# Kernel tuning notes

Measured on AMD Instinct MI355X. Metric: run time of the kernel, lower is better.

Reference implementation:

```python
import jax, jax.numpy as jnp
import numpy as np
from jax import lax

V, E, H, SEQ = 50257, 512, 512, 2048
TAGS, START, STOP = 12, 10, 11
NEG = -10000.0


def _lstm_dir(x, Wih, Whh, bih, bhh, reverse):
    # x: [T, in], Wih: [4H, in], Whh: [4H, H] (torch gate order i,f,g,o)
    h0 = jnp.zeros((Whh.shape[1],), x.dtype)
    c0 = jnp.zeros((Whh.shape[1],), x.dtype)
    b = bih + bhh

    def step(carry, xt):
        h, c = carry
        gates = Wih @ xt + Whh @ h + b  # [4H]
        i, f, g, o = jnp.split(gates, 4)
        c = jax.nn.sigmoid(f) * c + jax.nn.sigmoid(i) * jnp.tanh(g)
        h = jax.nn.sigmoid(o) * jnp.tanh(c)
        return (h, c), h

    _, hs = lax.scan(step, (h0, c0), x, reverse=reverse)
    return hs  # [T, H]


def _bilstm_layer(x, Wih, Whh, bih, bhh):
    # stacked params: leading dim 2 = (fwd, bwd)
    fwd = _lstm_dir(x, Wih[0], Whh[0], bih[0], bhh[0], False)
    bwd = _lstm_dir(x, Wih[1], Whh[1], bih[1], bhh[1], True)
    return jnp.concatenate([fwd, bwd], axis=-1)  # [T, 2H]


def _viterbi(feats, transitions):
    # feats: [T, TAGS]; transitions[next, prev]
    init = jnp.full((TAGS,), NEG, feats.dtype).at[START].set(0.0)

    def step(fv, feat):
        scores = fv[None, :] + transitions  # [next, prev]
        bptr = jnp.argmax(scores, axis=1)
        fv_new = jnp.max(scores, axis=1) + feat
        return fv_new, bptr

    fv, bptrs = lax.scan(step, init, feats)
    terminal = fv + transitions[STOP]
    best_last = jnp.argmax(terminal)
    path_score = terminal[best_last]

    def back(tag, bp):
        prev = bp[tag]
        return prev, prev

    _, ys = lax.scan(back, best_last, bptrs, reverse=True)
    # ys[t] = path[t-1]; ys[0] = START (dropped); append best_last
    best_path = jnp.concatenate([ys[1:], best_last[None]])
    return path_score, best_path


def setup_inputs() -> dict:
    key = jax.random.key(0)
    ks = jax.random.split(key, 16)
    s = lambda *sh: 1.0 / np.sqrt(H)
    inp = {
        "sentence": jax.random.randint(ks[0], (SEQ,), 0, V),
        "emb": jax.random.normal(ks[1], (V, E), jnp.float32),
        "Wih0": jax.random.uniform(ks[2], (2, 4 * H, E), jnp.float32, -s(), s()),
        "Whh0": jax.random.uniform(ks[3], (2, 4 * H, H), jnp.float32, -s(), s()),
        "bih0": jax.random.uniform(ks[4], (2, 4 * H), jnp.float32, -s(), s()),
        "bhh0": jax.random.uniform(ks[5], (2, 4 * H), jnp.float32, -s(), s()),
        "Wih1": jax.random.uniform(ks[6], (2, 4 * H, 2 * H), jnp.float32, -s(), s()),
        "Whh1": jax.random.uniform(ks[7], (2, 4 * H, H), jnp.float32, -s(), s()),
        "bih1": jax.random.uniform(ks[8], (2, 4 * H), jnp.float32, -s(), s()),
        "bhh1": jax.random.uniform(ks[9], (2, 4 * H), jnp.float32, -s(), s()),
        "W_tag": jax.random.uniform(ks[10], (TAGS, 2 * H), jnp.float32, -0.1, 0.1),
        "b_tag": jnp.zeros((TAGS,), jnp.float32),
    }
    trans = jax.random.normal(ks[11], (TAGS, TAGS), jnp.float32)
    trans = trans.at[START, :].set(NEG).at[:, STOP].set(NEG)
    inp["transitions"] = trans
    return inp


def reference(sentence, emb, Wih0, Whh0, bih0, bhh0, Wih1, Whh1, bih1, bhh1, W_tag, b_tag, transitions):
    x = emb[sentence]  # [T, E]  (dropout identity in eval)
    x = _bilstm_layer(x, Wih0, Whh0, bih0, bhh0)
    x = _bilstm_layer(x, Wih1, Whh1, bih1, bhh1)
    feats = x @ W_tag.T + b_tag  # [T, TAGS]
    path_score, best_path = _viterbi(feats, transitions)
    return path_score, best_path
```

## Files before the change

### kernel.cpp

```cpp
#include <hip/hip_runtime.h>
#include <math.h>

#define SEQ 2048
#define EMB_D 512
#define HID 512
#define NTAGS 12
#define START_TAG 10
#define STOP_TAG 11
#define NEGV (-10000.0f)
#define POISON 0xAAAAAAAAu

__device__ __forceinline__ float sigf(float x) { return 1.0f / (1.0f + expf(-x)); }

__global__ void k_embed(const int* __restrict__ sent, const float* __restrict__ emb,
                        float* __restrict__ x0) {
    int t = blockIdx.x;
    int tid = threadIdx.x;
    int row = sent[t];
    const float4* src = (const float4*)(emb + (size_t)row * EMB_D);
    float4* dst = (float4*)(x0 + (size_t)t * EMB_D);
    dst[tid] = src[tid];
}

#define BM 64
#define BN 64
#define BKT 32
#define LDT 68

__global__ __launch_bounds__(256) void k_gemm(
    const float* __restrict__ Af, const float* __restrict__ Ab,
    const float* __restrict__ B,
    const float* __restrict__ biasA, const float* __restrict__ biasB,
    float* __restrict__ C, int K) {
    const int N = 2048;
    int dir = blockIdx.z;
    const float* Bd = B + (size_t)dir * N * K;
    const float* bA = biasA + dir * N;
    const float* bB = biasB + dir * N;
    float* Cd = C + (size_t)dir * 2048 * N;
    int m0 = blockIdx.y * BM, n0 = blockIdx.x * BN;

    __shared__ float As[BKT * LDT];
    __shared__ float Bs[BKT * LDT];

    int tid = threadIdx.x;
    int lrow = tid >> 2;
    int lk4 = (tid & 3) * 8;
    int tx = tid & 15, ty = tid >> 4;

    float acc[4][4] = {};

    for (int kt = 0; kt < K; kt += BKT) {
        {
            int m = m0 + lrow;
#pragma unroll
            for (int hh = 0; hh < 2; ++hh) {
                int k = kt + lk4 + hh * 4;
                const float* src = (k < 512) ? (Af + (size_t)m * 512 + k)
                                             : (Ab + (size_t)m * 512 + (k - 512));
                float4 v = *(const float4*)src;
                int kl = lk4 + hh * 4;
                As[(kl + 0) * LDT + lrow] = v.x;
                As[(kl + 1) * LDT + lrow] = v.y;
                As[(kl + 2) * LDT + lrow] = v.z;
                As[(kl + 3) * LDT + lrow] = v.w;
            }
        }
        {
            int n = n0 + lrow;
#pragma unroll
            for (int hh = 0; hh < 2; ++hh) {
                int k = kt + lk4 + hh * 4;
                float4 v = *(const float4*)(Bd + (size_t)n * K + k);
                int kl = lk4 + hh * 4;
                Bs[(kl + 0) * LDT + lrow] = v.x;
                Bs[(kl + 1) * LDT + lrow] = v.y;
                Bs[(kl + 2) * LDT + lrow] = v.z;
                Bs[(kl + 3) * LDT + lrow] = v.w;
            }
        }
        __syncthreads();
#pragma unroll
        for (int kk = 0; kk < BKT; ++kk) {
            float4 av = *(const float4*)&As[kk * LDT + ty * 4];
            float4 bv = *(const float4*)&Bs[kk * LDT + tx * 4];
            acc[0][0] += av.x * bv.x; acc[0][1] += av.x * bv.y; acc[0][2] += av.x * bv.z; acc[0][3] += av.x * bv.w;
            acc[1][0] += av.y * bv.x; acc[1][1] += av.y * bv.y; acc[1][2] += av.y * bv.z; acc[1][3] += av.y * bv.w;
            acc[2][0] += av.z * bv.x; acc[2][1] += av.z * bv.y; acc[2][2] += av.z * bv.z; acc[2][3] += av.z * bv.w;
            acc[3][0] += av.w * bv.x; acc[3][1] += av.w * bv.y; acc[3][2] += av.w * bv.z; acc[3][3] += av.w * bv.w;
        }
        __syncthreads();
    }
#pragma unroll
    for (int i = 0; i < 4; ++i) {
        int m = m0 + ty * 4 + i;
#pragma unroll
        for (int j = 0; j < 4; ++j) {
            int n = n0 + tx * 4 + j;
            Cd[(size_t)m * N + n] = acc[i][j] + bA[n] + bB[n];
        }
    }
}

#define HPAD 132

__global__ __launch_bounds__(256, 1) void k_lstm(
    const float* __restrict__ Whh,
    const float* __restrict__ Gi,
    float* __restrict__ hstore)
{
    int wg = blockIdx.x;
    int dir = wg >> 5;
    int slice = wg & 31;
    int u_base = slice * 16;
    int tid = threadIdx.x;

    const float* Whh_d = Whh + (size_t)dir * 2048 * 512;
    const float* Gi_d = Gi + (size_t)dir * 2048 * 2048;
    float* h_d = hstore + (size_t)dir * 2048 * 512;

    int rl = tid >> 2;
    int kp = tid & 3;
    int gg = rl >> 4;
    int uu = rl & 15;
    int r = gg * 512 + u_base + uu;

    float w[128];
    {
        const float* wsrc = Whh_d + (size_t)r * 512 + kp * 128;
#pragma unroll
        for (int j = 0; j < 128; j += 4) {
            float4 v = *(const float4*)(wsrc + j);
            w[j] = v.x; w[j + 1] = v.y; w[j + 2] = v.z; w[j + 3] = v.w;
        }
    }

    __shared__ __align__(16) float hlds[4 * HPAD];
    __shared__ float gdot[64];
    float c_reg = 0.0f;

    int sec = tid >> 6;
    int soff = (tid & 63) * 2;
    float* hstage = hlds + sec * HPAD + soff;

    for (int it = 0; it < 2048; ++it) {
        int t = dir ? (2047 - it) : it;

        float gi = 0.f;
        if (kp == 0) gi = Gi_d[(size_t)t * 2048 + r];

        if (it == 0) {
            hstage[0] = 0.f;
            hstage[1] = 0.f;
        } else {
            int tprev = dir ? (t + 1) : (t - 1);
            const unsigned long long* src =
                (const unsigned long long*)(h_d + (size_t)tprev * 512) + tid;
            unsigned long long v;
            do {
                v = __hip_atomic_load(src, __ATOMIC_RELAXED, __HIP_MEMORY_SCOPE_AGENT);
            } while ((unsigned)v == POISON || (unsigned)(v >> 32) == POISON);
            hstage[0] = __uint_as_float((unsigned)v);
            hstage[1] = __uint_as_float((unsigned)(v >> 32));
        }
        __syncthreads();

        float p = 0.f;
        const float4* h4 = (const float4*)(hlds + kp * HPAD);
#pragma unroll
        for (int j4 = 0; j4 < 32; ++j4) {
            float4 hv = h4[j4];
            p += w[4 * j4 + 0] * hv.x;
            p += w[4 * j4 + 1] * hv.y;
            p += w[4 * j4 + 2] * hv.z;
            p += w[4 * j4 + 3] * hv.w;
        }
        p += __shfl_xor(p, 1);
        p += __shfl_xor(p, 2);
        if (kp == 0) {
            float v = p + gi;
            gdot[rl] = (gg == 2) ? tanhf(v) : sigf(v);
        }
        __syncthreads();

        if (tid < 16) {
            float iv = gdot[0 * 16 + tid];
            float fv = gdot[1 * 16 + tid];
            float gv = gdot[2 * 16 + tid];
            float ov = gdot[3 * 16 + tid];
            float c = fv * c_reg + iv * gv;
            float h = ov * tanhf(c);
            c_reg = c;
            __hip_atomic_store(h_d + (size_t)t * 512 + u_base + tid, h,
                               __ATOMIC_RELAXED, __HIP_MEMORY_SCOPE_AGENT);
        }
    }
}

__global__ __launch_bounds__(64) void k_feats(
    const float* __restrict__ h1,
    const float* __restrict__ Wt,
    const float* __restrict__ bt,
    float* __restrict__ feats)
{
    int t = blockIdx.x;
    int lane = threadIdx.x;
    __shared__ __align__(16) float xl[1024];
    const float4* hf = (const float4*)(h1 + (size_t)t * 512);
    const float4* hb = (const float4*)(h1 + (size_t)(2048 + t) * 512);
    ((float4*)xl)[lane] = hf[lane];
    ((float4*)xl)[lane + 64] = hf[lane + 64];
    ((float4*)xl)[128 + lane] = hb[lane];
    ((float4*)xl)[128 + lane + 64] = hb[lane + 64];
    __syncthreads();
    for (int tag = 0; tag < NTAGS; ++tag) {
        const float* wrow = Wt + tag * 1024;
        float s = 0.f;
        for (int k = lane; k < 1024; k += 64) s += xl[k] * wrow[k];
#pragma unroll
        for (int off = 32; off; off >>= 1) s += __shfl_xor(s, off);
        if (lane == 0) feats[t * NTAGS + tag] = s + bt[tag];
    }
}

__global__ __launch_bounds__(64) void k_viterbi(
    const float* __restrict__ feats, const float* __restrict__ trans,
    float* __restrict__ out) {
    __shared__ float fv[2][NTAGS];
    __shared__ unsigned char bp[SEQ * NTAGS];
    __shared__ float featbuf[256 * NTAGS];
    __shared__ float term[NTAGS];
    int lane = threadIdx.x;

    float tr[NTAGS];
    if (lane < NTAGS) {
#pragma unroll
        for (int p = 0; p < NTAGS; ++p) tr[p] = trans[lane * NTAGS + p];
        fv[0][lane] = (lane == START_TAG) ? 0.f : NEGV;
    }
    __syncthreads();

    int cur = 0;
    for (int tc = 0; tc < SEQ; tc += 256) {
        for (int i = lane; i < 256 * NTAGS; i += 64) featbuf[i] = feats[tc * NTAGS + i];
        __syncthreads();
        for (int tt = 0; tt < 256; ++tt) {
            int t = tc + tt;
            if (lane < NTAGS) {
                float best = fv[cur][0] + tr[0];
                int bi = 0;
#pragma unroll
                for (int p = 1; p < NTAGS; ++p) {
                    float s = fv[cur][p] + tr[p];
                    if (s > best) { best = s; bi = p; }
                }
                bp[t * NTAGS + lane] = (unsigned char)bi;
                fv[cur ^ 1][lane] = best + featbuf[tt * NTAGS + lane];
            }
            cur ^= 1;
            __syncthreads();
        }
    }

    if (lane < NTAGS) term[lane] = fv[cur][lane] + trans[STOP_TAG * NTAGS + lane];
    __syncthreads();
    if (lane == 0) {
        float best = term[0];
        int bi = 0;
        for (int p = 1; p < NTAGS; ++p) {
            if (term[p] > best) { best = term[p]; bi = p; }
        }
        out[0] = best;
        int tag = bi;
        out[1 + (SEQ - 1)] = (float)tag;
        for (int t = SEQ - 1; t >= 1; --t) {
            tag = bp[t * NTAGS + tag];
            out[t] = (float)tag;
        }
    }
}

extern "C" void kernel_launch(void* const* d_in, const int* in_sizes, int n_in,
                              void* d_out, int out_size, void* d_ws, size_t ws_size,
                              hipStream_t stream) {
    const int* sent = (const int*)d_in[0];
    const float* emb = (const float*)d_in[1];
    const float* Wih0 = (const float*)d_in[2];
    const float* Whh0 = (const float*)d_in[3];
    const float* bih0 = (const float*)d_in[4];
    const float* bhh0 = (const float*)d_in[5];
    const float* Wih1 = (const float*)d_in[6];
    const float* Whh1 = (const float*)d_in[7];
    const float* bih1 = (const float*)d_in[8];
    const float* bhh1 = (const float*)d_in[9];
    const float* Wtag = (const float*)d_in[10];
    const float* btag = (const float*)d_in[11];
    const float* trans = (const float*)d_in[12];
    float* out = (float*)d_out;

    char* ws = (char*)d_ws;
    size_t off = 0;
    auto alloc = [&](size_t bytes) {
        void* p = ws + off;
        off += (bytes + 255) & ~(size_t)255;
        return p;
    };
    float* x0 = (float*)alloc(2048ull * 512 * 4);
    float* Gi = (float*)alloc(2ull * 2048 * 2048 * 4);
    float* h0 = (float*)alloc(2ull * 2048 * 512 * 4);
    float* h1 = (float*)alloc(2ull * 2048 * 512 * 4);
    float* feats = (float*)alloc(2048ull * NTAGS * 4);

    hipMemsetAsync(h0, 0xAA, 2ull * 2048 * 512 * 4, stream);
    hipMemsetAsync(h1, 0xAA, 2ull * 2048 * 512 * 4, stream);

    k_embed<<<2048, 128, 0, stream>>>(sent, emb, x0);

    dim3 gg(32, 32, 2);
    k_gemm<<<gg, 256, 0, stream>>>(x0, x0, Wih0, bih0, bhh0, Gi, 512);
    k_lstm<<<64, 256, 0, stream>>>(Whh0, Gi, h0);
    k_gemm<<<gg, 256, 0, stream>>>(h0, h0 + 2048ull * 512, Wih1, bih1, bhh1, Gi, 1024);
    k_lstm<<<64, 256, 0, stream>>>(Whh1, Gi, h1);
    k_feats<<<2048, 64, 0, stream>>>(h1, Wtag, btag, feats);
    k_viterbi<<<1, 64, 0, stream>>>(feats, trans, out);
}
```

Measured before the change: 8.902 ms.

## Enlarge GEMM tiles to 128x128 with 8x8 per-thread blocking; pin LSTM weights; backoff polling

The input-projection GEMM moves from 64x64 tiles with 4x4 per-thread outputs to 128x128 tiles with 8x8 per-thread outputs and a K-step of 16, which raises arithmetic intensity per shared-memory load. The LSTM kernel adds empty asm constraints so the 128 weight registers stay resident in VGPRs rather than being spilled or rematerialised. The spin-wait on the previous timestep's hidden state now inserts s_sleep between polls, which reduces memory traffic from polling but may add wake-up latency on the serial critical path. The GEMM grid shrinks to 512 blocks, and occupancy drops because of higher register pressure.

```diff
diff --git a/kernel.cpp b/kernel.cpp
--- a/kernel.cpp
+++ b/kernel.cpp
@@ -22,10 +22,10 @@
     dst[tid] = src[tid];
 }
 
-#define BM 64
-#define BN 64
-#define BKT 32
-#define LDT 68
+#define GBM 128
+#define GBN 128
+#define GBK 16
+#define GLD 132
 
 __global__ __launch_bounds__(256) void k_gemm(
     const float* __restrict__ Af, const float* __restrict__ Ab,
@@ -38,65 +38,70 @@
     const float* bA = biasA + dir * N;
     const float* bB = biasB + dir * N;
     float* Cd = C + (size_t)dir * 2048 * N;
-    int m0 = blockIdx.y * BM, n0 = blockIdx.x * BN;
-
-    __shared__ float As[BKT * LDT];
-    __shared__ float Bs[BKT * LDT];
+    int m0 = blockIdx.y * GBM, n0 = blockIdx.x * GBN;
+
+    __shared__ float As[GBK * GLD];
+    __shared__ float Bs[GBK * GLD];
 
     int tid = threadIdx.x;
-    int lrow = tid >> 2;
-    int lk4 = (tid & 3) * 8;
+    int lrow = tid >> 1;
+    int lk = (tid & 1) * 8;
     int tx = tid & 15, ty = tid >> 4;
 
-    float acc[4][4] = {};
-
-    for (int kt = 0; kt < K; kt += BKT) {
+    float acc[8][8] = {};
+
+    for (int kt = 0; kt < K; kt += GBK) {
         {
             int m = m0 + lrow;
-#pragma unroll
-            for (int hh = 0; hh < 2; ++hh) {
-                int k = kt + lk4 + hh * 4;
-                const float* src = (k < 512) ? (Af + (size_t)m * 512 + k)
-                                             : (Ab + (size_t)m * 512 + (k - 512));
-                float4 v = *(const float4*)src;
-                int kl = lk4 + hh * 4;
-                As[(kl + 0) * LDT + lrow] = v.x;
-                As[(kl + 1) * LDT + lrow] = v.y;
-                As[(kl + 2) * LDT + lrow] = v.z;
-                As[(kl + 3) * LDT + lrow] = v.w;
-            }
+            const float* base = (kt < 512) ? (Af + (size_t)m * 512 + kt)
+                                           : (Ab + (size_t)m * 512 + (kt - 512));
+            float4 v0 = *(const float4*)(base + lk);
+            float4 v1 = *(const float4*)(base + lk + 4);
+            As[(lk + 0) * GLD + lrow] = v0.x;
+            As[(lk + 1) * GLD + lrow] = v0.y;
+            As[(lk + 2) * GLD + lrow] = v0.z;
+            As[(lk + 3) * GLD + lrow] = v0.w;
+            As[(lk + 4) * GLD + lrow] = v1.x;
+            As[(lk + 5) * GLD + lrow] = v1.y;
+            As[(lk + 6) * GLD + lrow] = v1.z;
+            As[(lk + 7) * GLD + lrow] = v1.w;
         }
         {
             int n = n0 + lrow;
-#pragma unroll
-            for (int hh = 0; hh < 2; ++hh) {
-                int k = kt + lk4 + hh * 4;
-                float4 v = *(const float4*)(Bd + (size_t)n * K + k);
-                int kl = lk4 + hh * 4;
-                Bs[(kl + 0) * LDT + lrow] = v.x;
-                Bs[(kl + 1) * LDT + lrow] = v.y;
-                Bs[(kl + 2) * LDT + lrow] = v.z;
-                Bs[(kl + 3) * LDT + lrow] = v.w;
-            }
-        }
-        __syncthreads();
-#pragma unroll
-        for (int kk = 0; kk < BKT; ++kk) {
-            float4 av = *(const float4*)&As[kk * LDT + ty * 4];
-            float4 bv = *(const float4*)&Bs[kk * LDT + tx * 4];
-            acc[0][0] += av.x * bv.x; acc[0][1] += av.x * bv.y; acc[0][2] += av.x * bv.z; acc[0][3] += av.x * bv.w;
-            acc[1][0] += av.y * bv.x; acc[1][1] += av.y * bv.y; acc[1][2] += av.y * bv.z; acc[1][3] += av.y * bv.w;
-            acc[2][0] += av.z * bv.x; acc[2][1] += av.z * bv.y; acc[2][2] += av.z * bv.z; acc[2][3] += av.z * bv.w;
-            acc[3][0] += av.w * bv.x; acc[3][1] += av.w * bv.y; acc[3][2] += av.w * bv.z; acc[3][3] += av.w * bv.w;
-        }
-        __syncthreads();
-    }
-#pragma unroll
-    for (int i = 0; i < 4; ++i) {
-        int m = m0 + ty * 4 + i;
-#pragma unroll
-        for (int j = 0; j < 4; ++j) {
-            int n = n0 + tx * 4 + j;
+            const float* base = Bd + (size_t)n * K + kt;
+            float4 v0 = *(const float4*)(base + lk);
+            float4 v1 = *(const float4*)(base + lk + 4);
+            Bs[(lk + 0) * GLD + lrow] = v0.x;
+            Bs[(lk + 1) * GLD + lrow] = v0.y;
+            Bs[(lk + 2) * GLD + lrow] = v0.z;
+            Bs[(lk + 3) * GLD + lrow] = v0.w;
+            Bs[(lk + 4) * GLD + lrow] = v1.x;
+            Bs[(lk + 5) * GLD + lrow] = v1.y;
+            Bs[(lk + 6) * GLD + lrow] = v1.z;
+            Bs[(lk + 7) * GLD + lrow] = v1.w;
+        }
+        __syncthreads();
+#pragma unroll
+        for (int kk = 0; kk < GBK; ++kk) {
+            float4 a0 = *(const float4*)&As[kk * GLD + ty * 8];
+            float4 a1 = *(const float4*)&As[kk * GLD + ty * 8 + 4];
+            float4 b0 = *(const float4*)&Bs[kk * GLD + tx * 8];
+            float4 b1 = *(const float4*)&Bs[kk * GLD + tx * 8 + 4];
+            float av[8] = {a0.x, a0.y, a0.z, a0.w, a1.x, a1.y, a1.z, a1.w};
+            float bv[8] = {b0.x, b0.y, b0.z, b0.w, b1.x, b1.y, b1.z, b1.w};
+#pragma unroll
+            for (int i = 0; i < 8; ++i)
+#pragma unroll
+                for (int j = 0; j < 8; ++j) acc[i][j] += av[i] * bv[j];
+        }
+        __syncthreads();
+    }
+#pragma unroll
+    for (int i = 0; i < 8; ++i) {
+        int m = m0 + ty * 8 + i;
+#pragma unroll
+        for (int j = 0; j < 8; ++j) {
+            int n = n0 + tx * 8 + j;
             Cd[(size_t)m * N + n] = acc[i][j] + bA[n] + bB[n];
         }
     }
@@ -134,6 +139,9 @@
             w[j] = v.x; w[j + 1] = v.y; w[j + 2] = v.z; w[j + 3] = v.w;
         }
     }
+#pragma unroll
+    for (int j = 0; j < 128; j += 4)
+        asm volatile("" : "+v"(w[j]), "+v"(w[j + 1]), "+v"(w[j + 2]), "+v"(w[j + 3]));
 
     __shared__ __align__(16) float hlds[4 * HPAD];
     __shared__ float gdot[64];
@@ -156,10 +164,12 @@
             int tprev = dir ? (t + 1) : (t - 1);
             const unsigned long long* src =
                 (const unsigned long long*)(h_d + (size_t)tprev * 512) + tid;
-            unsigned long long v;
-            do {
+            unsigned long long v =
+                __hip_atomic_load(src, __ATOMIC_RELAXED, __HIP_MEMORY_SCOPE_AGENT);
+            while ((unsigned)v == POISON || (unsigned)(v >> 32) == POISON) {
+                __builtin_amdgcn_s_sleep(1);
                 v = __hip_atomic_load(src, __ATOMIC_RELAXED, __HIP_MEMORY_SCOPE_AGENT);
-            } while ((unsigned)v == POISON || (unsigned)(v >> 32) == POISON);
+            }
             hstage[0] = __uint_as_float((unsigned)v);
             hstage[1] = __uint_as_float((unsigned)(v >> 32));
         }
@@ -316,7 +326,7 @@
 
     k_embed<<<2048, 128, 0, stream>>>(sent, emb, x0);
 
-    dim3 gg(32, 32, 2);
+    dim3 gg(16, 16, 2);
     k_gemm<<<gg, 256, 0, stream>>>(x0, x0, Wih0, bih0, bhh0, Gi, 512);
     k_lstm<<<64, 256, 0, stream>>>(Whh0, Gi, h0);
     k_gemm<<<gg, 256, 0, stream>>>(h0, h0 + 2048ull * 512, Wih1, bih1, bhh1, Gi, 1024);
```

Measured after the change: 9.444 ms. +6.1%, slower.
